# Performance work log

Measured on AMD Instinct MI355X. Metric: run time of the kernel, lower is better.

The kernel has to match this reference:

```python
import jax, jax.numpy as jnp
import numpy as np

NI = 512
HEADS = 8
DH = NI // HEADS  # 64 = attn_chans
EPS = 1e-5

def _ln(x, g, b):
    mu = jnp.mean(x, axis=-1, keepdims=True)
    var = jnp.var(x, axis=-1, keepdims=True)
    return (x - mu) * jax.lax.rsqrt(var + EPS) * g + b

def setup_inputs() -> dict:
    key = jax.random.key(0)
    ks = jax.random.split(key, 5)
    n, c, h, w = 8, NI, 32, 32
    return {
        "x": jax.random.normal(ks[0], (n, c, h, w), jnp.float32),
        "query_x": jax.random.normal(ks[1], (n, c, h, w), jnp.float32),
        "q_ln_g": jnp.ones((c,), jnp.float32),
        "q_ln_b": jnp.zeros((c,), jnp.float32),
        "q_w": jax.random.normal(ks[2], (c, c), jnp.float32) / np.sqrt(c),
        "q_b": jnp.zeros((c,), jnp.float32),
        "kv_ln_g": jnp.ones((c,), jnp.float32),
        "kv_ln_b": jnp.zeros((c,), jnp.float32),
        "kv_w": jax.random.normal(ks[3], (c, 2 * c), jnp.float32) / np.sqrt(c),
        "kv_b": jnp.zeros((2 * c,), jnp.float32),
        "proj_w": jax.random.normal(ks[4], (c, c), jnp.float32) / np.sqrt(c),
        "proj_b": jnp.zeros((c,), jnp.float32),
    }

def reference(x, query_x, q_ln_g, q_ln_b, q_w, q_b, kv_ln_g, kv_ln_b, kv_w, kv_b, proj_w, proj_b):
    n, c, h, w = x.shape
    s = h * w
    xs = x.reshape(n, c, s).transpose(0, 2, 1)        # (n, s, c)
    qx = query_x.reshape(n, c, s).transpose(0, 2, 1)  # (n, s, c)
    q_proj = _ln(qx, q_ln_g, q_ln_b) @ q_w + q_b        # (n, s, c)
    kv = _ln(xs, kv_ln_g, kv_ln_b) @ kv_w + kv_b        # (n, s, 2c)
    cat = jnp.concatenate([q_proj, kv], axis=-1)        # (n, s, 3c)
    # rearrange 'n s (h d3)' with h=HEADS, d3 = 3*DH, then chunk into q,k,v
    cat = cat.reshape(n, s, HEADS, 3 * DH).transpose(0, 2, 1, 3)  # (n, H, s, 3d)
    q, k, v = jnp.split(cat, 3, axis=-1)                # each (n, H, s, d)
    scale = jnp.sqrt(jnp.asarray(DH, q.dtype))          # sqrt(ni/nheads)
    scores = jnp.einsum('nhqd,nhkd->nhqk', q, k) / scale
    attn = jax.nn.softmax(scores, axis=-1)
    o = jnp.einsum('nhqk,nhkd->nhqd', attn, v)          # (n, H, s, d)
    o = o.transpose(0, 2, 1, 3).reshape(n, s, c)        # (n, s, c)
    o = o @ proj_w + proj_b
    return o.transpose(0, 2, 1).reshape(n, c, h, w)
```

## Files before the change

### kernel.cpp

```cpp
#include <hip/hip_runtime.h>
#include <math.h>

namespace {

constexpr int S = 1024;
constexpr int C = 512;
constexpr int NBATCH = 8;
constexpr int RTOT = NBATCH * S;
constexpr int HEADS = 8;
constexpr int DH = 64;

typedef __attribute__((ext_vector_type(8))) short bf16x8;
typedef __attribute__((ext_vector_type(4))) float f32x4;
typedef __attribute__((ext_vector_type(16))) float f32x16;
typedef unsigned short u16;
typedef unsigned int u32;

__device__ __forceinline__ u16 f2bf(float x) {
  union { float f; u32 u; } v; v.f = x;
  u32 r = v.u + 0x7FFF + ((v.u >> 16) & 1);
  return (u16)(r >> 16);
}
__device__ __forceinline__ float bf2f(u16 b) {
  union { u32 u; float f; } v; v.u = (u32)b << 16; return v.f;
}
__device__ __forceinline__ u32 cvtpk(float a, float b) {
  u32 r;
  asm("v_cvt_pk_bf16_f32 %0, %1, %2" : "=v"(r) : "v"(a), "v"(b));
  return r;
}
__device__ __forceinline__ void gl_lds16(const void* g, void* l) {
  auto gp = (const __attribute__((address_space(1))) u32*)g;
  auto lp = (__attribute__((address_space(3))) u32*)l;
  __builtin_amdgcn_global_load_lds(gp, lp, 16, 0, 0);
}

__global__ void ln_fused(const float* __restrict__ x, const float* __restrict__ qx,
                         const float* __restrict__ gx, const float* __restrict__ bx,
                         const float* __restrict__ gq, const float* __restrict__ bq,
                         u16* __restrict__ Xkv, u16* __restrict__ Xq) {
  __shared__ float Ssum[8][32], Ssq[8][32];
  __shared__ float mu_s[32], rs_s[32];
  __shared__ float T[32][65];
  int t = threadIdx.x;
  int si0 = blockIdx.x * 32;
  int isq = blockIdx.y & 1, n = blockIdx.y >> 1;
  const float* in = isq ? qx : x;
  const float* g  = isq ? gq : gx;
  const float* be = isq ? bq : bx;
  u16* out = isq ? Xq : Xkv;

  {
    int sl = t & 31, cg = t >> 5;
    const float* p = in + ((size_t)n * C + cg * 64) * S + si0 + sl;
    float s = 0.f, sq = 0.f;
#pragma unroll 8
    for (int c = 0; c < 64; c++) { float v = p[(size_t)c * S]; s += v; sq += v * v; }
    Ssum[cg][sl] = s; Ssq[cg][sl] = sq;
  }
  __syncthreads();
  if (t < 32) {
    float ss = 0.f, q2 = 0.f;
#pragma unroll
    for (int i = 0; i < 8; i++) { ss += Ssum[i][t]; q2 += Ssq[i][t]; }
    float m = ss * (1.0f / C);
    float var = q2 * (1.0f / C) - m * m;
    mu_s[t] = m; rs_s[t] = rsqrtf(var + 1e-5f);
  }
  __syncthreads();

  int si4 = (t & 7) * 4, cl = t >> 3;
  float4 mu4 = *(const float4*)&mu_s[si4];
  float4 rs4 = *(const float4*)&rs_s[si4];
  int wsl = t >> 3, wc8 = (t & 7) * 8;

  for (int c0 = 0; c0 < C; c0 += 64) {
#pragma unroll
    for (int i = 0; i < 2; i++) {
      int c = c0 + cl + i * 32;
      float4 v = *(const float4*)&in[((size_t)n * C + c) * S + si0 + si4];
      float gg = g[c], bb = be[c];
      T[si4 + 0][cl + i * 32] = (v.x - mu4.x) * rs4.x * gg + bb;
      T[si4 + 1][cl + i * 32] = (v.y - mu4.y) * rs4.y * gg + bb;
      T[si4 + 2][cl + i * 32] = (v.z - mu4.z) * rs4.z * gg + bb;
      T[si4 + 3][cl + i * 32] = (v.w - mu4.w) * rs4.w * gg + bb;
    }
    __syncthreads();
    u16 pk[8];
#pragma unroll
    for (int j = 0; j < 8; j++) pk[j] = f2bf(T[wsl][wc8 + j]);
    *(uint4*)&out[((size_t)(n * S + si0 + wsl)) * C + c0 + wc8] = *(const uint4*)pk;
    __syncthreads();
  }
}

__global__ void prep_w(const float* __restrict__ qw, const float* __restrict__ kvw,
                       const float* __restrict__ pw,
                       u16* __restrict__ Wtq, u16* __restrict__ Wtkv,
                       u16* __restrict__ Wph, u16* __restrict__ Wpl) {
  int z = blockIdx.z;
  int N = (z == 1) ? 1024 : 512;
  int col0 = blockIdx.y * 64;
  if (col0 >= N) return;
  int k0 = blockIdx.x * 64;
  const float* W = (z == 0) ? qw : (z == 1) ? kvw : pw;
  __shared__ float T[64][65];
  int t = threadIdx.x;
  int kl = t >> 4, c4 = (t & 15) * 4;
#pragma unroll
  for (int i = 0; i < 4; i++) {
    float4 v = *(const float4*)&W[(size_t)(k0 + kl + i * 16) * N + col0 + c4];
    T[kl + i * 16][c4 + 0] = v.x; T[kl + i * 16][c4 + 1] = v.y;
    T[kl + i * 16][c4 + 2] = v.z; T[kl + i * 16][c4 + 3] = v.w;
  }
  __syncthreads();
#pragma unroll
  for (int p = 0; p < 2; p++) {
    int cl = (t >> 3) + p * 32, k8 = (t & 7) * 8;
    u16 hi[8], lo[8];
#pragma unroll
    for (int j = 0; j < 8; j++) {
      float f = T[k8 + j][cl];
      u16 hv = f2bf(f);
      hi[j] = hv;
      lo[j] = f2bf(f - bf2f(hv));
    }
    size_t o = (size_t)(col0 + cl) * 512 + k0 + k8;
    if (z == 0) *(uint4*)&Wtq[o] = *(const uint4*)hi;
    else if (z == 1) *(uint4*)&Wtkv[o] = *(const uint4*)hi;
    else { *(uint4*)&Wph[o] = *(const uint4*)hi; *(uint4*)&Wpl[o] = *(const uint4*)lo; }
  }
}

__global__ __launch_bounds__(256, 4) void gemm_qkv(
    const u16* __restrict__ Xq, const u16* __restrict__ Xkv,
    const u16* __restrict__ Wtq, const u16* __restrict__ Wtkv,
    const float* __restrict__ q_b, const float* __restrict__ kv_b,
    u16* __restrict__ Qb, u16* __restrict__ Kb, u16* __restrict__ Vt) {
  __shared__ __attribute__((aligned(16))) u16 As[128 * 64];
  __shared__ __attribute__((aligned(16))) u16 Bs[128 * 64];
  int t = threadIdx.x, wid = t >> 6, lane = t & 63, lr = lane & 15, lg = lane >> 4;
  int colb = blockIdx.x;
  const u16* A; const u16* Wt; const float* bias; int ch0;
  if (colb < 4) { A = Xq;  Wt = Wtq  + (size_t)colb * 128 * 512;       bias = q_b  + colb * 128;       ch0 = colb * 128; }
  else          { A = Xkv; Wt = Wtkv + (size_t)(colb - 4) * 128 * 512; bias = kv_b + (colb - 4) * 128; ch0 = 512 + (colb - 4) * 128; }
  int row0 = blockIdx.y * 128;
  int wr = wid >> 1, wc = wid & 1;
  f32x4 acc[4][4];
#pragma unroll
  for (int m = 0; m < 4; m++)
#pragma unroll
    for (int n = 0; n < 4; n++) acc[m][n] = (f32x4){0.f, 0.f, 0.f, 0.f};

  for (int k0 = 0; k0 < 512; k0 += 64) {
    __syncthreads();
#pragma unroll
    for (int it = 0; it < 4; it++) {
      int chunk = (wid * 4 + it) * 64 + lane;
      int r = chunk >> 3, sg = chunk & 7;
      gl_lds16(A + (size_t)(row0 + r) * 512 + k0 + ((sg ^ (r & 7)) * 8),
               (char*)As + (size_t)chunk * 16);
    }
#pragma unroll
    for (int it = 0; it < 4; it++) {
      int chunk = (wid * 4 + it) * 64 + lane;
      int r = chunk >> 3, sg = chunk & 7;
      gl_lds16(Wt + (size_t)r * 512 + k0 + ((sg ^ (r & 7)) * 8),
               (char*)Bs + (size_t)chunk * 16);
    }
    __syncthreads();
#pragma unroll
    for (int kk = 0; kk < 2; kk++) {
      bf16x8 bfr[4];
#pragma unroll
      for (int n = 0; n < 4; n++) {
        int col = wc * 64 + n * 16 + lr;
        bfr[n] = *(const bf16x8*)((const char*)Bs + col * 128 + (((kk * 4 + lg) ^ (col & 7)) << 4));
      }
#pragma unroll
      for (int m = 0; m < 4; m++) {
        int row = wr * 64 + m * 16 + lr;
        bf16x8 af = *(const bf16x8*)((const char*)As + row * 128 + (((kk * 4 + lg) ^ (row & 7)) << 4));
#pragma unroll
        for (int n = 0; n < 4; n++)
          acc[m][n] = __builtin_amdgcn_mfma_f32_16x16x32_bf16(af, bfr[n], acc[m][n], 0, 0, 0);
      }
    }
  }
#pragma unroll
  for (int m = 0; m < 4; m++)
#pragma unroll
    for (int n = 0; n < 4; n++) {
      int colg = wc * 64 + n * 16 + lr;
      int ch = ch0 + colg;
      int h = ch / 192, role = (ch >> 6) % 3, d = ch & 63;
      float bs = bias[colg];
      float qsc = (role == 0) ? 0.18033688f : 1.0f;
      int growb = row0 + wr * 64 + m * 16 + lg * 4;
      int nn = growb >> 10, ssi0 = growb & (S - 1);
      size_t nh = (size_t)(nn * HEADS + h);
      if (role == 2) {
        u16 pk[4];
#pragma unroll
        for (int r = 0; r < 4; r++) pk[r] = f2bf(acc[m][n][r] + bs);
        *(uint2*)&Vt[(nh * DH + d) * S + ssi0] = *(const uint2*)pk;
      } else {
        u16* dst = (role == 0) ? Qb : Kb;
#pragma unroll
        for (int r = 0; r < 4; r++)
          dst[(nh * S + ssi0 + r) * DH + d] = f2bf((acc[m][n][r] + bs) * qsc);
      }
    }
}

__global__ __launch_bounds__(256) void gemm_proj(
    const u16* __restrict__ Aob, const u16* __restrict__ Wh, const u16* __restrict__ Wl,
    const float* __restrict__ bias, float* __restrict__ out) {
  __shared__ __attribute__((aligned(16))) u16 As[128 * 64];
  __shared__ __attribute__((aligned(16))) u16 Bh[64 * 64];
  __shared__ __attribute__((aligned(16))) u16 Bl[64 * 64];
  int t = threadIdx.x, wid = t >> 6, lane = t & 63, lr = lane & 15, lg = lane >> 4;
  int ch0 = blockIdx.x * 64, row0 = blockIdx.y * 128;
  int wc = wid & 1, wr = wid >> 1;
  f32x4 acc[2][4];
#pragma unroll
  for (int m = 0; m < 2; m++)
#pragma unroll
    for (int n = 0; n < 4; n++) acc[m][n] = (f32x4){0.f, 0.f, 0.f, 0.f};

  for (int k0 = 0; k0 < 512; k0 += 64) {
    __syncthreads();
#pragma unroll
    for (int it = 0; it < 4; it++) {
      int idx = (wid * 4 + it) * 64 + lane;
      int r = idx >> 3, sg = idx & 7;
      gl_lds16(Aob + (size_t)(row0 + r) * 512 + k0 + ((sg ^ (r & 7)) * 8),
               (char*)As + (wid * 4 + it) * 1024);
    }
#pragma unroll
    for (int it = 0; it < 2; it++) {
      int idx = (wid * 2 + it) * 64 + lane;
      int r = idx >> 3, sg = idx & 7;
      size_t go = (size_t)(ch0 + r) * 512 + k0 + ((sg ^ (r & 7)) * 8);
      gl_lds16(Wh + go, (char*)Bh + (wid * 2 + it) * 1024);
      gl_lds16(Wl + go, (char*)Bl + (wid * 2 + it) * 1024);
    }
    __syncthreads();
#pragma unroll
    for (int kk = 0; kk < 2; kk++) {
      bf16x8 ar[4];
#pragma unroll
      for (int n = 0; n < 4; n++) {
        int row = wr * 64 + n * 16 + lr;
        ar[n] = *(const bf16x8*)((const char*)As + row * 128 + (((kk * 4 + lg) ^ (row & 7)) << 4));
      }
#pragma unroll
      for (int m = 0; m < 2; m++) {
        int ch = wc * 32 + m * 16 + lr;
        bf16x8 bh = *(const bf16x8*)((const char*)Bh + ch * 128 + (((kk * 4 + lg) ^ (ch & 7)) << 4));
        bf16x8 bl = *(const bf16x8*)((const char*)Bl + ch * 128 + (((kk * 4 + lg) ^ (ch & 7)) << 4));
#pragma unroll
        for (int n = 0; n < 4; n++) {
          acc[m][n] = __builtin_amdgcn_mfma_f32_16x16x32_bf16(bh, ar[n], acc[m][n], 0, 0, 0);
          acc[m][n] = __builtin_amdgcn_mfma_f32_16x16x32_bf16(bl, ar[n], acc[m][n], 0, 0, 0);
        }
      }
    }
  }
#pragma unroll
  for (int m = 0; m < 2; m++)
#pragma unroll
    for (int n = 0; n < 4; n++) {
      int rowg = row0 + wr * 64 + n * 16 + lr;
      int nn = rowg >> 10, ssi = rowg & (S - 1);
#pragma unroll
      for (int r = 0; r < 4; r++) {
        int ch = ch0 + wc * 32 + m * 16 + lg * 4 + r;
        out[((size_t)nn * C + ch) * S + ssi] = acc[m][n][r] + bias[ch];
      }
    }
}

constexpr int KVB = 64;

__global__ __launch_bounds__(256, 4) void attn_kernel(
    const u16* __restrict__ Qbf, const u16* __restrict__ Kbf,
    const u16* __restrict__ Vtb, u16* __restrict__ Obf) {
  __shared__ __attribute__((aligned(16))) u16 Ks[2][KVB * DH];
  __shared__ __attribute__((aligned(16))) u16 Vs[2][DH * KVB];

  int tid = threadIdx.x;
  int wave = tid >> 6, lane = tid & 63;
  int lq = lane & 31, hi = lane >> 5;
  int qg = wave & 1, kg = wave >> 1;
  int w = (blockIdx.x & 7) * 128 + (blockIdx.x >> 3);
  int qt = w & 15, nh = w >> 4;
  const u16* Qg = Qbf + (size_t)nh * S * DH;
  const u16* Kg = Kbf + (size_t)nh * S * DH;
  const u16* Vg = Vtb + (size_t)nh * DH * S;

  int qrow = qt * 64 + qg * 32 + lq;
  bf16x8 qf[4];
#pragma unroll
  for (int ks = 0; ks < 4; ks++)
    qf[ks] = *(const bf16x8*)(Qg + (size_t)qrow * DH + ks * 16 + hi * 8);

  f32x16 oa0 = {}, oa1 = {};
  float m_run = -1e30f, l_run = 0.f;

  int e0i = tid, e1i = tid + 256;
  int r0 = e0i >> 3, sg0 = e0i & 7, r1 = e1i >> 3, sg1 = e1i & 7;
  char* kd0 = (char*)&Ks[0][0] + (e0i & ~63) * 16;
  char* kd1 = (char*)&Ks[0][0] + (e1i & ~63) * 16;
  char* vd0 = (char*)&Vs[0][0] + (e0i & ~63) * 16;
  char* vd1 = (char*)&Vs[0][0] + (e1i & ~63) * 16;

#define STAGE(kb, b)                                                             \
  do {                                                                           \
    gl_lds16(Kg + (size_t)((kb) * KVB + r0) * 64 + ((sg0 ^ (r0 & 7)) * 8),       \
             kd0 + (b) * (KVB * DH * 2));                                        \
    gl_lds16(Kg + (size_t)((kb) * KVB + r1) * 64 + ((sg1 ^ (r1 & 7)) * 8),       \
             kd1 + (b) * (KVB * DH * 2));                                        \
    gl_lds16(Vg + (size_t)r0 * S + (kb) * KVB + ((sg0 ^ (r0 & 7)) * 8),          \
             vd0 + (b) * (KVB * DH * 2));                                        \
    gl_lds16(Vg + (size_t)r1 * S + (kb) * KVB + ((sg1 ^ (r1 & 7)) * 8),          \
             vd1 + (b) * (KVB * DH * 2));                                        \
  } while (0)

  STAGE(0, 0);

  for (int kb = 0; kb < S / KVB; kb++) {
    int cur = kb & 1;
    __syncthreads();
    if (kb + 1 < S / KVB) STAGE(kb + 1, cur ^ 1);

    const char* Kc = (const char*)&Ks[cur][0];
    const char* Vc = (const char*)&Vs[cur][0];

    f32x16 sc = {};
#pragma unroll
    for (int ks = 0; ks < 4; ks++) {
      int sg = ks * 2 + hi;
      bf16x8 kf = *(const bf16x8*)(Kc + (kg * 32 + lq) * 128 + ((sg ^ (lq & 7)) << 4));
      sc = __builtin_amdgcn_mfma_f32_32x32x16_bf16(kf, qf[ks], sc, 0, 0, 0);
    }

    float mx[8];
#pragma unroll
    for (int r = 0; r < 8; r++) mx[r] = fmaxf(sc[2 * r], sc[2 * r + 1]);
#pragma unroll
    for (int r = 0; r < 4; r++) mx[r] = fmaxf(mx[r], mx[r + 4]);
    float pmax = fmaxf(fmaxf(mx[0], mx[1]), fmaxf(mx[2], mx[3]));
    pmax = fmaxf(pmax, __shfl_xor(pmax, 32));

    if (!__all(pmax <= m_run + 11.5f)) {
      float mnew = fmaxf(m_run, pmax);
      float corr = exp2f(m_run - mnew);
      m_run = mnew;
      l_run *= corr;
#pragma unroll
      for (int r = 0; r < 16; r++) { oa0[r] *= corr; oa1[r] *= corr; }
    }

#pragma unroll
    for (int r = 0; r < 16; r++) sc[r] = exp2f(sc[r] - m_run);
    {
      float s8[8];
#pragma unroll
      for (int r = 0; r < 8; r++) s8[r] = sc[2 * r] + sc[2 * r + 1];
#pragma unroll
      for (int r = 0; r < 4; r++) s8[r] += s8[r + 4];
      float psum = (s8[0] + s8[1]) + (s8[2] + s8[3]);
      psum += __shfl_xor(psum, 32);
      l_run += psum;
    }

    u32 c[8];
    c[0] = cvtpk(sc[0],  sc[1]);  c[1] = cvtpk(sc[2],  sc[3]);
    c[2] = cvtpk(sc[4],  sc[5]);  c[3] = cvtpk(sc[6],  sc[7]);
    c[4] = cvtpk(sc[8],  sc[9]);  c[5] = cvtpk(sc[10], sc[11]);
    c[6] = cvtpk(sc[12], sc[13]); c[7] = cvtpk(sc[14], sc[15]);
    asm("v_permlane32_swap_b32 %0, %1" : "+v"(c[0]), "+v"(c[2]));
    asm("v_permlane32_swap_b32 %0, %1" : "+v"(c[1]), "+v"(c[3]));
    asm("v_permlane32_swap_b32 %0, %1" : "+v"(c[4]), "+v"(c[6]));
    asm("v_permlane32_swap_b32 %0, %1" : "+v"(c[5]), "+v"(c[7]));

#pragma unroll
    for (int kk = 0; kk < 2; kk++) {
      union { u32 u[4]; bf16x8 v; } pu;
      pu.u[0] = c[kk * 4 + 0]; pu.u[1] = c[kk * 4 + 1];
      pu.u[2] = c[kk * 4 + 2]; pu.u[3] = c[kk * 4 + 3];
      int sg = kg * 4 + kk * 2 + hi;
      bf16x8 vf0 = *(const bf16x8*)(Vc + lq * 128 + ((sg ^ (lq & 7)) << 4));
      bf16x8 vf1 = *(const bf16x8*)(Vc + (32 + lq) * 128 + ((sg ^ (lq & 7)) << 4));
      oa0 = __builtin_amdgcn_mfma_f32_32x32x16_bf16(vf0, pu.v, oa0, 0, 0, 0);
      oa1 = __builtin_amdgcn_mfma_f32_32x32x16_bf16(vf1, pu.v, oa1, 0, 0, 0);
    }
  }
#undef STAGE

  __syncthreads();
  float* exO = (float*)&Ks[0][0];
  float* exS = (float*)&Vs[0][0];
  if (kg) {
    float* o = exO + qg * 2048;
#pragma unroll
    for (int r = 0; r < 16; r++) {
      o[r * 64 + lane] = oa0[r];
      o[(16 + r) * 64 + lane] = oa1[r];
    }
    exS[qg * 128 + lane] = m_run;
    exS[qg * 128 + 64 + lane] = l_run;
  }
  __syncthreads();
  if (!kg) {
    float* o = exO + qg * 2048;
    float m2 = exS[qg * 128 + lane];
    float l2 = exS[qg * 128 + 64 + lane];
    float m = fmaxf(m_run, m2);
    float f0 = exp2f(m_run - m), f2 = exp2f(m2 - m);
    l_run = l_run * f0 + l2 * f2;
#pragma unroll
    for (int r = 0; r < 16; r++) {
      oa0[r] = oa0[r] * f0 + o[r * 64 + lane] * f2;
      oa1[r] = oa1[r] * f0 + o[(16 + r) * 64 + lane] * f2;
    }
    int n = nh >> 3, h = nh & 7;
    float lf = 1.0f / l_run;
    u16* orow = Obf + ((size_t)n * S + qrow) * C + h * DH;
#pragma unroll
    for (int rq = 0; rq < 4; rq++) {
      int d0 = rq * 8 + 4 * hi;
      uint2 w0, w1;
      w0.x = cvtpk(oa0[rq * 4 + 0] * lf, oa0[rq * 4 + 1] * lf);
      w0.y = cvtpk(oa0[rq * 4 + 2] * lf, oa0[rq * 4 + 3] * lf);
      w1.x = cvtpk(oa1[rq * 4 + 0] * lf, oa1[rq * 4 + 1] * lf);
      w1.y = cvtpk(oa1[rq * 4 + 2] * lf, oa1[rq * 4 + 3] * lf);
      *(uint2*)(orow + d0) = w0;
      *(uint2*)(orow + 32 + d0) = w1;
    }
  }
}

}

extern "C" void kernel_launch(void* const* d_in, const int* in_sizes, int n_in,
                              void* d_out, int out_size, void* d_ws, size_t ws_size,
                              hipStream_t stream) {
  const float* x       = (const float*)d_in[0];
  const float* qx      = (const float*)d_in[1];
  const float* q_ln_g  = (const float*)d_in[2];
  const float* q_ln_b  = (const float*)d_in[3];
  const float* q_w     = (const float*)d_in[4];
  const float* q_b     = (const float*)d_in[5];
  const float* kv_ln_g = (const float*)d_in[6];
  const float* kv_ln_b = (const float*)d_in[7];
  const float* kv_w    = (const float*)d_in[8];
  const float* kv_b    = (const float*)d_in[9];
  const float* proj_w  = (const float*)d_in[10];
  const float* proj_b  = (const float*)d_in[11];
  float* out = (float*)d_out;

  u16* u = (u16*)d_ws;
  u16* Xkv  = u;                u += (size_t)RTOT * C;
  u16* Xq   = u;                u += (size_t)RTOT * C;
  u16* Wtq  = u;                u += (size_t)C * C;
  u16* Wtkv = u;                u += (size_t)2 * C * C;
  u16* Wph  = u;                u += (size_t)C * C;
  u16* Wpl  = u;                u += (size_t)C * C;
  u16* Qb   = u;                u += (size_t)NBATCH * HEADS * S * DH;
  u16* Kb   = u;                u += (size_t)NBATCH * HEADS * S * DH;
  u16* Vt   = u;                u += (size_t)NBATCH * HEADS * S * DH;
  u16* Obf  = u;

  hipLaunchKernelGGL(ln_fused, dim3(S / 32, 2 * NBATCH), dim3(256), 0, stream,
                     x, qx, kv_ln_g, kv_ln_b, q_ln_g, q_ln_b, Xkv, Xq);
  hipLaunchKernelGGL(prep_w, dim3(8, 16, 3), dim3(256), 0, stream,
                     q_w, kv_w, proj_w, Wtq, Wtkv, Wph, Wpl);
  hipLaunchKernelGGL(gemm_qkv, dim3(12, RTOT / 128), dim3(256), 0, stream,
                     Xq, Xkv, Wtq, Wtkv, q_b, kv_b, Qb, Kb, Vt);
  hipLaunchKernelGGL(attn_kernel, dim3(1024), dim3(256), 0, stream,
                     Qb, Kb, Vt, Obf);
  hipLaunchKernelGGL(gemm_proj, dim3(C / 64, RTOT / 128), dim3(256), 0, stream,
                     Obf, Wph, Wpl, proj_b, out);
}
```

Measured before the change: 95.73 us.

## Load K/V directly from global per wave and split keys into halves

Drops the shared-memory double-buffered K/V staging in the attention kernel. Each key-group wave now reads its K and V fragments straight from global memory over a contiguous half of the sequence, instead of both key groups interleaving 32-row slices of each 64-row tile. This removes per-iteration barriers and LDS traffic, but relies on L2/cache for reuse across the two query-group waves and exposes global load latency with no explicit prefetch. It also swaps exp2f for the hardware exp2 intrinsic.

```diff
diff --git a/kernel.cpp b/kernel.cpp
--- a/kernel.cpp
+++ b/kernel.cpp
@@ -281,13 +281,11 @@
     }
 }
 
-constexpr int KVB = 64;
-
 __global__ __launch_bounds__(256, 4) void attn_kernel(
     const u16* __restrict__ Qbf, const u16* __restrict__ Kbf,
     const u16* __restrict__ Vtb, u16* __restrict__ Obf) {
-  __shared__ __attribute__((aligned(16))) u16 Ks[2][KVB * DH];
-  __shared__ __attribute__((aligned(16))) u16 Vs[2][DH * KVB];
+  __shared__ float exO[2][32][64];
+  __shared__ float exS[2][2][64];
 
   int tid = threadIdx.x;
   int wave = tid >> 6, lane = tid & 63;
@@ -296,8 +294,8 @@
   int w = (blockIdx.x & 7) * 128 + (blockIdx.x >> 3);
   int qt = w & 15, nh = w >> 4;
   const u16* Qg = Qbf + (size_t)nh * S * DH;
-  const u16* Kg = Kbf + (size_t)nh * S * DH;
-  const u16* Vg = Vtb + (size_t)nh * DH * S;
+  const u16* Kg = Kbf + (size_t)nh * S * DH + (size_t)(kg * 512) * DH;
+  const u16* Vg = Vtb + (size_t)nh * DH * S + kg * 512;
 
   int qrow = qt * 64 + qg * 32 + lq;
   bf16x8 qf[4];
@@ -308,42 +306,24 @@
   f32x16 oa0 = {}, oa1 = {};
   float m_run = -1e30f, l_run = 0.f;
 
-  int e0i = tid, e1i = tid + 256;
-  int r0 = e0i >> 3, sg0 = e0i & 7, r1 = e1i >> 3, sg1 = e1i & 7;
-  char* kd0 = (char*)&Ks[0][0] + (e0i & ~63) * 16;
-  char* kd1 = (char*)&Ks[0][0] + (e1i & ~63) * 16;
-  char* vd0 = (char*)&Vs[0][0] + (e0i & ~63) * 16;
-  char* vd1 = (char*)&Vs[0][0] + (e1i & ~63) * 16;
-
-#define STAGE(kb, b)                                                             \
-  do {                                                                           \
-    gl_lds16(Kg + (size_t)((kb) * KVB + r0) * 64 + ((sg0 ^ (r0 & 7)) * 8),       \
-             kd0 + (b) * (KVB * DH * 2));                                        \
-    gl_lds16(Kg + (size_t)((kb) * KVB + r1) * 64 + ((sg1 ^ (r1 & 7)) * 8),       \
-             kd1 + (b) * (KVB * DH * 2));                                        \
-    gl_lds16(Vg + (size_t)r0 * S + (kb) * KVB + ((sg0 ^ (r0 & 7)) * 8),          \
-             vd0 + (b) * (KVB * DH * 2));                                        \
-    gl_lds16(Vg + (size_t)r1 * S + (kb) * KVB + ((sg1 ^ (r1 & 7)) * 8),          \
-             vd1 + (b) * (KVB * DH * 2));                                        \
-  } while (0)
-
-  STAGE(0, 0);
-
-  for (int kb = 0; kb < S / KVB; kb++) {
-    int cur = kb & 1;
-    __syncthreads();
-    if (kb + 1 < S / KVB) STAGE(kb + 1, cur ^ 1);
-
-    const char* Kc = (const char*)&Ks[cur][0];
-    const char* Vc = (const char*)&Vs[cur][0];
+  for (int t = 0; t < 16; t++) {
+    const u16* Kt = Kg + (size_t)(t * 32) * DH;
+    bf16x8 kf0 = *(const bf16x8*)(Kt + (size_t)lq * DH + 0 * 16 + hi * 8);
+    bf16x8 kf1 = *(const bf16x8*)(Kt + (size_t)lq * DH + 1 * 16 + hi * 8);
+    bf16x8 kf2 = *(const bf16x8*)(Kt + (size_t)lq * DH + 2 * 16 + hi * 8);
+    bf16x8 kf3 = *(const bf16x8*)(Kt + (size_t)lq * DH + 3 * 16 + hi * 8);
+    const u16* Vt0 = Vg + (size_t)lq * S + t * 32 + hi * 8;
+    const u16* Vt1 = Vg + (size_t)(32 + lq) * S + t * 32 + hi * 8;
+    bf16x8 vf00 = *(const bf16x8*)(Vt0);
+    bf16x8 vf01 = *(const bf16x8*)(Vt0 + 16);
+    bf16x8 vf10 = *(const bf16x8*)(Vt1);
+    bf16x8 vf11 = *(const bf16x8*)(Vt1 + 16);
 
     f32x16 sc = {};
-#pragma unroll
-    for (int ks = 0; ks < 4; ks++) {
-      int sg = ks * 2 + hi;
-      bf16x8 kf = *(const bf16x8*)(Kc + (kg * 32 + lq) * 128 + ((sg ^ (lq & 7)) << 4));
-      sc = __builtin_amdgcn_mfma_f32_32x32x16_bf16(kf, qf[ks], sc, 0, 0, 0);
-    }
+    sc = __builtin_amdgcn_mfma_f32_32x32x16_bf16(kf0, qf[0], sc, 0, 0, 0);
+    sc = __builtin_amdgcn_mfma_f32_32x32x16_bf16(kf1, qf[1], sc, 0, 0, 0);
+    sc = __builtin_amdgcn_mfma_f32_32x32x16_bf16(kf2, qf[2], sc, 0, 0, 0);
+    sc = __builtin_amdgcn_mfma_f32_32x32x16_bf16(kf3, qf[3], sc, 0, 0, 0);
 
     float mx[8];
 #pragma unroll
@@ -355,7 +335,7 @@
 
     if (!__all(pmax <= m_run + 11.5f)) {
       float mnew = fmaxf(m_run, pmax);
-      float corr = exp2f(m_run - mnew);
+      float corr = __builtin_amdgcn_exp2f(m_run - mnew);
       m_run = mnew;
       l_run *= corr;
 #pragma unroll
@@ -363,7 +343,7 @@
     }
 
 #pragma unroll
-    for (int r = 0; r < 16; r++) sc[r] = exp2f(sc[r] - m_run);
+    for (int r = 0; r < 16; r++) sc[r] = __builtin_amdgcn_exp2f(sc[r] - m_run);
     {
       float s8[8];
 #pragma unroll
@@ -385,45 +365,38 @@
     asm("v_permlane32_swap_b32 %0, %1" : "+v"(c[4]), "+v"(c[6]));
     asm("v_permlane32_swap_b32 %0, %1" : "+v"(c[5]), "+v"(c[7]));
 
-#pragma unroll
-    for (int kk = 0; kk < 2; kk++) {
+    {
       union { u32 u[4]; bf16x8 v; } pu;
-      pu.u[0] = c[kk * 4 + 0]; pu.u[1] = c[kk * 4 + 1];
-      pu.u[2] = c[kk * 4 + 2]; pu.u[3] = c[kk * 4 + 3];
-      int sg = kg * 4 + kk * 2 + hi;
-      bf16x8 vf0 = *(const bf16x8*)(Vc + lq * 128 + ((sg ^ (lq & 7)) << 4));
-      bf16x8 vf1 = *(const bf16x8*)(Vc + (32 + lq) * 128 + ((sg ^ (lq & 7)) << 4));
-      oa0 = __builtin_amdgcn_mfma_f32_32x32x16_bf16(vf0, pu.v, oa0, 0, 0, 0);
-      oa1 = __builtin_amdgcn_mfma_f32_32x32x16_bf16(vf1, pu.v, oa1, 0, 0, 0);
-    }
-  }
-#undef STAGE
+      pu.u[0] = c[0]; pu.u[1] = c[1]; pu.u[2] = c[2]; pu.u[3] = c[3];
+      oa0 = __builtin_amdgcn_mfma_f32_32x32x16_bf16(vf00, pu.v, oa0, 0, 0, 0);
+      oa1 = __builtin_amdgcn_mfma_f32_32x32x16_bf16(vf10, pu.v, oa1, 0, 0, 0);
+      pu.u[0] = c[4]; pu.u[1] = c[5]; pu.u[2] = c[6]; pu.u[3] = c[7];
+      oa0 = __builtin_amdgcn_mfma_f32_32x32x16_bf16(vf01, pu.v, oa0, 0, 0, 0);
+      oa1 = __builtin_amdgcn_mfma_f32_32x32x16_bf16(vf11, pu.v, oa1, 0, 0, 0);
+    }
+  }
 
   __syncthreads();
-  float* exO = (float*)&Ks[0][0];
-  float* exS = (float*)&Vs[0][0];
   if (kg) {
-    float* o = exO + qg * 2048;
 #pragma unroll
     for (int r = 0; r < 16; r++) {
-      o[r * 64 + lane] = oa0[r];
-      o[(16 + r) * 64 + lane] = oa1[r];
-    }
-    exS[qg * 128 + lane] = m_run;
-    exS[qg * 128 + 64 + lane] = l_run;
+      exO[qg][r][lane] = oa0[r];
+      exO[qg][16 + r][lane] = oa1[r];
+    }
+    exS[qg][0][lane] = m_run;
+    exS[qg][1][lane] = l_run;
   }
   __syncthreads();
   if (!kg) {
-    float* o = exO + qg * 2048;
-    float m2 = exS[qg * 128 + lane];
-    float l2 = exS[qg * 128 + 64 + lane];
+    float m2 = exS[qg][0][lane];
+    float l2 = exS[qg][1][lane];
     float m = fmaxf(m_run, m2);
-    float f0 = exp2f(m_run - m), f2 = exp2f(m2 - m);
+    float f0 = __builtin_amdgcn_exp2f(m_run - m), f2 = __builtin_amdgcn_exp2f(m2 - m);
     l_run = l_run * f0 + l2 * f2;
 #pragma unroll
     for (int r = 0; r < 16; r++) {
-      oa0[r] = oa0[r] * f0 + o[r * 64 + lane] * f2;
-      oa1[r] = oa1[r] * f0 + o[(16 + r) * 64 + lane] * f2;
+      oa0[r] = oa0[r] * f0 + exO[qg][r][lane] * f2;
+      oa1[r] = oa1[r] * f0 + exO[qg][16 + r][lane] * f2;
     }
     int n = nh >> 3, h = nh & 7;
     float lf = 1.0f / l_run;
```

Result: slower. 121.5 us (+27.0%).
